# Kernel tuning notes

Measured on AMD Instinct MI355X. Metric: run time of the kernel, lower is better.

The kernel has to match this reference:

```python
import jax, jax.numpy as jnp
import numpy as np

B, T, C, HS = 4, 4096, 1024, 128

def setup_inputs() -> dict:
    key = jax.random.key(0)
    kx, kq, kk, kv = jax.random.split(key, 4)
    x = jax.random.normal(kx, (B, T, C), dtype=jnp.float32)
    # bias-free Linear weights, stored as (in, out) so projection is x @ W
    scale = 1.0 / np.sqrt(C)
    Wq = jax.random.normal(kq, (C, HS), dtype=jnp.float32) * scale
    Wk = jax.random.normal(kk, (C, HS), dtype=jnp.float32) * scale
    Wv = jax.random.normal(kv, (C, HS), dtype=jnp.float32) * scale
    return {"x": x, "Wq": Wq, "Wk": Wk, "Wv": Wv}

def reference(x, Wq, Wk, Wv):
    # x: (B,T,C) -> q,k,v: (B,T,HS)
    q = jnp.einsum('btc,ch->bth', x, Wq)
    k = jnp.einsum('btc,ch->bth', x, Wk)
    v = jnp.einsum('btc,ch->bth', x, Wv)
    hs = k.shape[-1]
    # scaled scores (B,T,T) with causal mask
    wei = jnp.einsum('bth,bsh->bts', q, k) * (hs ** -0.5)
    causal = jnp.tril(jnp.ones((q.shape[1], q.shape[1]), dtype=bool))
    wei = jnp.where(causal, wei, -jnp.inf)
    wei = jax.nn.softmax(wei, axis=-1)
    # dropout p=0.0 -> identity
    out = jnp.einsum('bts,bsh->bth', wei, v)
    return out
```

## Files before the change

### kernel.cpp

```cpp
#include <hip/hip_runtime.h>
#include <hip/hip_bf16.h>

typedef __attribute__((ext_vector_type(8))) short short8;
typedef __attribute__((ext_vector_type(4))) short s4v;
typedef __attribute__((ext_vector_type(4))) float f32x4;

#define BATCH 4
#define TLEN 4096
#define CDIM 1024
#define HSD 128
#define MROWS (BATCH*TLEN)

#define QSCALE 0.12751744f

#ifdef __HIP_DEVICE_COMPILE__
  #define MFMA16(a,b,c) __builtin_amdgcn_mfma_f32_16x16x16bf16_1k(a,b,c,0,0,0)
#else
  #define MFMA16(a,b,c) (c)
#endif

__device__ __forceinline__ unsigned short f2bf(float f){
    unsigned u = __builtin_bit_cast(unsigned, f);
    u = (u + 0x7FFFu + ((u >> 16) & 1u)) >> 16;
    return (unsigned short)u;
}
__device__ __forceinline__ unsigned pkbf(float a, float b){
    unsigned ua = (__builtin_bit_cast(unsigned, a) + 0x8000u) >> 16;
    unsigned ub = (__builtin_bit_cast(unsigned, b) + 0x8000u) & 0xFFFF0000u;
    return ua | ub;
}

__global__ void prep_w_k(const float* __restrict__ Wq, const float* __restrict__ Wk,
                         const float* __restrict__ Wv, unsigned short* __restrict__ Wt){
    int idx = blockIdx.x * 256 + threadIdx.x;
    const int total = 3 * HSD * CDIM;
    if (idx >= total) return;
    int w = idx / (HSD * CDIM);
    int r = idx - w * HSD * CDIM;
    int h = r / CDIM;
    int c = r - h * CDIM;
    const float* W = (w == 0) ? Wq : ((w == 1) ? Wk : Wv);
    Wt[idx] = f2bf(W[c * HSD + h]);
}

__device__ __forceinline__ void stage_w_tile(unsigned short* buf, const unsigned short* g,
                                             int tid){
#pragma unroll
    for (int i = 0; i < 2; i++){
        int c = i * 256 + tid;
        int row = c >> 2, kp = c & 3;
        int swz = (row & 3) ^ ((row >> 2) & 3);
        const unsigned short* gp = g + (size_t)row * CDIM + ((kp ^ swz) << 3);
        unsigned short* lp = buf + (c << 3);
        __builtin_amdgcn_global_load_lds((const __attribute__((address_space(1))) void*)gp,
                                         (__attribute__((address_space(3))) void*)lp, 16, 0, 0);
    }
}

__global__ __launch_bounds__(256) void proj_k(const float* __restrict__ x,
                                              const unsigned short* __restrict__ Wt,
                                              unsigned short* __restrict__ Qb,
                                              unsigned short* __restrict__ Kb,
                                              unsigned short* __restrict__ Vt){
    __shared__ unsigned short As[2][64 * 32];
    __shared__ unsigned short Bs[2][128 * 32];

    const int tid = threadIdx.x, lane = tid & 63, wave = tid >> 6;
    const int m = lane & 15, quad = lane >> 4;
    const int wr = wave & 1, wc = wave >> 1;
    const int rb = blockIdx.x * 64;
    const int p  = blockIdx.y;

    const float* gA = x + (size_t)rb * CDIM;
    const unsigned short* gB = Wt + (size_t)(p * HSD) * CDIM;

    const int arow = tid >> 2, ach = tid & 3;
    const int aswz = (arow & 3) ^ ((arow >> 2) & 3);
    const int agc = ach ^ aswz;
    const float* agp = gA + (size_t)arow * CDIM + (agc << 3);

    f32x4 acc[4][4];
#pragma unroll
    for (int i = 0; i < 4; i++)
#pragma unroll
        for (int j = 0; j < 4; j++) acc[i][j] = (f32x4)0.f;

    stage_w_tile(&Bs[0][0], gB, tid);
    {
        float4 a0 = *(const float4*)(agp);
        float4 a1 = *(const float4*)(agp + 4);
        short8 o;
        o[0]=(short)f2bf(a0.x); o[1]=(short)f2bf(a0.y); o[2]=(short)f2bf(a0.z); o[3]=(short)f2bf(a0.w);
        o[4]=(short)f2bf(a1.x); o[5]=(short)f2bf(a1.y); o[6]=(short)f2bf(a1.z); o[7]=(short)f2bf(a1.w);
        *(short8*)&As[0][arow * 32 + (ach << 3)] = o;
    }
    __syncthreads();

    int cur = 0;
    for (int kc = 0; kc < CDIM / 32; ++kc){
        float4 a0n, a1n;
        if (kc + 1 < CDIM / 32){
            stage_w_tile(&Bs[cur ^ 1][0], gB + (kc + 1) * 32, tid);
            a0n = *(const float4*)(agp + (kc + 1) * 32);
            a1n = *(const float4*)(agp + (kc + 1) * 32 + 4);
        }
        if (p < 2){
            short8 aF[4], bF[2];
#pragma unroll
            for (int i = 0; i < 4; i++){
                int ra = wr * 64 + i * 16 + m;
                int sa = (ra & 3) ^ ((ra >> 2) & 3);
                aF[i] = *(const short8*)&Bs[cur][ra * 32 + ((quad ^ sa) << 3)];
            }
#pragma unroll
            for (int j = 0; j < 2; j++){
                int rn = wc * 32 + j * 16 + m;
                int sb = (rn & 3) ^ ((rn >> 2) & 3);
                bF[j] = *(const short8*)&As[cur][rn * 32 + ((quad ^ sb) << 3)];
            }
#pragma unroll
            for (int i = 0; i < 4; i++)
#pragma unroll
                for (int j = 0; j < 2; j++)
                    acc[i][j] = __builtin_amdgcn_mfma_f32_16x16x32_bf16(aF[i], bF[j], acc[i][j], 0, 0, 0);
        } else {
            short8 aF[2], bF[4];
#pragma unroll
            for (int i = 0; i < 2; i++){
                int ra = wr * 32 + i * 16 + m;
                int sa = (ra & 3) ^ ((ra >> 2) & 3);
                aF[i] = *(const short8*)&As[cur][ra * 32 + ((quad ^ sa) << 3)];
            }
#pragma unroll
            for (int j = 0; j < 4; j++){
                int rn = wc * 64 + j * 16 + m;
                int sb = (rn & 3) ^ ((rn >> 2) & 3);
                bF[j] = *(const short8*)&Bs[cur][rn * 32 + ((quad ^ sb) << 3)];
            }
#pragma unroll
            for (int i = 0; i < 2; i++)
#pragma unroll
                for (int j = 0; j < 4; j++)
                    acc[i][j] = __builtin_amdgcn_mfma_f32_16x16x32_bf16(aF[i], bF[j], acc[i][j], 0, 0, 0);
        }
        if (kc + 1 < CDIM / 32){
            short8 o;
            o[0]=(short)f2bf(a0n.x); o[1]=(short)f2bf(a0n.y); o[2]=(short)f2bf(a0n.z); o[3]=(short)f2bf(a0n.w);
            o[4]=(short)f2bf(a1n.x); o[5]=(short)f2bf(a1n.y); o[6]=(short)f2bf(a1n.z); o[7]=(short)f2bf(a1n.w);
            *(short8*)&As[cur ^ 1][arow * 32 + (ach << 3)] = o;
        }
        __syncthreads();
        cur ^= 1;
    }

    if (p < 2){
        unsigned short* D = (p == 0) ? Qb : Kb;
        const float qs = (p == 0) ? QSCALE : 1.0f;
#pragma unroll
        for (int i = 0; i < 4; i++){
#pragma unroll
            for (int j = 0; j < 2; j++){
                int h = wr * 64 + i * 16 + quad * 4;
                int t = rb + wc * 32 + j * 16 + m;
                ushort4 v;
                v.x = f2bf(acc[i][j][0] * qs); v.y = f2bf(acc[i][j][1] * qs);
                v.z = f2bf(acc[i][j][2] * qs); v.w = f2bf(acc[i][j][3] * qs);
                *(ushort4*)(D + (size_t)t * HSD + h) = v;
            }
        }
    } else {
        int b = rb >> 12;
        int tb = rb & 4095;
#pragma unroll
        for (int i = 0; i < 2; i++){
#pragma unroll
            for (int j = 0; j < 4; j++){
                int t = tb + wr * 32 + i * 16 + quad * 4;
                int h = wc * 64 + j * 16 + m;
                ushort4 v;
                v.x = f2bf(acc[i][j][0]); v.y = f2bf(acc[i][j][1]);
                v.z = f2bf(acc[i][j][2]); v.w = f2bf(acc[i][j][3]);
                *(ushort4*)(Vt + ((size_t)b * HSD + h) * TLEN + t) = v;
            }
        }
    }
}

__device__ __forceinline__ void stage_k_tile(unsigned short* buf, const unsigned short* g,
                                             int tid){
#pragma unroll
    for (int i = 0; i < 2; i++){
        int slot = i * 512 + tid;
        int row = slot >> 4;
        int ch  = slot & 15;
        const unsigned short* gp = g + row * 128 + ((ch ^ (row & 15)) << 3);
        unsigned short* lp = buf + (slot << 3);
        __builtin_amdgcn_global_load_lds((const __attribute__((address_space(1))) void*)gp,
                                         (__attribute__((address_space(3))) void*)lp, 16, 0, 0);
    }
}
__device__ __forceinline__ void stage_v_tile(unsigned short* buf, const unsigned short* g,
                                             int tid){
#pragma unroll
    for (int i = 0; i < 2; i++){
        int slot = i * 512 + tid;
        int row = slot >> 3;
        int ch  = slot & 7;
        const unsigned short* gp = g + (size_t)row * TLEN + ((ch ^ (row & 7)) << 3);
        unsigned short* lp = buf + (slot << 3);
        __builtin_amdgcn_global_load_lds((const __attribute__((address_space(1))) void*)gp,
                                         (__attribute__((address_space(3))) void*)lp, 16, 0, 0);
    }
}

__global__ __launch_bounds__(512) void attn_k(const unsigned short* __restrict__ Qb,
                       const unsigned short* __restrict__ Kb,
                       const unsigned short* __restrict__ Vts,
                       float* __restrict__ Opart, float* __restrict__ lpart, int seglen){
    __shared__ unsigned short Kt[64 * 128];
    __shared__ unsigned short Vs[128 * 64];

    const int tid = threadIdx.x, lane = tid & 63, wave = tid >> 6;
    const int m = lane & 15, quad = lane >> 4;
    const int q0 = ((int)gridDim.x - 1 - (int)blockIdx.x) * 128;
    const int seg = blockIdx.y, b = blockIdx.z;
    const int g0 = seg * seglen;
    if (g0 >= q0 + 128) return;
    const int gend = min(g0 + seglen, q0 + 128);
    const int nT = (gend - g0) >> 6;

    const int q0w = q0 + wave * 16;
    const size_t rowg = (size_t)b * TLEN + q0w;

    short8 aQ[4];
#pragma unroll
    for (int kk = 0; kk < 4; kk++)
        aQ[kk] = *(const short8*)(Qb + (rowg + m) * HSD + kk * 32 + quad * 8);

    f32x4 accO[8];
#pragma unroll
    for (int i = 0; i < 8; i++) accO[i] = (f32x4)0.f;
    float lp = 0.f;

    const unsigned short* kbase = Kb + (size_t)b * TLEN * HSD;
    const unsigned short* vbase = Vts + (size_t)b * HSD * TLEN;

    for (int t = 0; t < nT; ++t){
        const int s0 = g0 + t * 64;
        stage_k_tile(&Kt[0], kbase + (size_t)s0 * HSD, tid);
        stage_v_tile(&Vs[0], vbase + s0, tid);
        __syncthreads();

        if (s0 <= q0w + 15){
            f32x4 S[4];
#pragma unroll
            for (int ns = 0; ns < 4; ns++){
                f32x4 sa = (f32x4)0.f;
#pragma unroll
                for (int kk = 0; kk < 4; kk++){
                    short8 bK = *(const short8*)&Kt[(ns * 16 + m) * 128 + (((kk * 4 + quad) ^ m) << 3)];
                    sa = __builtin_amdgcn_mfma_f32_16x16x32_bf16(bK, aQ[kk], sa, 0, 0, 0);
                }
                S[ns] = sa;
            }
            if (s0 + 63 > q0w){
                int qg = q0w + m;
#pragma unroll
                for (int ns = 0; ns < 4; ns++){
#pragma unroll
                    for (int r = 0; r < 4; r++){
                        int sg = s0 + ns * 16 + quad * 4 + r;
                        if (sg > qg) S[ns][r] = -1e30f;
                    }
                }
            }
            s4v aP[4];
#pragma unroll
            for (int ns = 0; ns < 4; ns++){
                float p0 = exp2f(S[ns][0]), p1 = exp2f(S[ns][1]);
                float p2 = exp2f(S[ns][2]), p3 = exp2f(S[ns][3]);
                lp += (p0 + p1) + (p2 + p3);
                uint2 u;
                u.x = pkbf(p0, p1);
                u.y = pkbf(p2, p3);
                aP[ns] = __builtin_bit_cast(s4v, u);
            }
#pragma unroll
            for (int sub = 0; sub < 8; sub++){
#pragma unroll
                for (int ns = 0; ns < 4; ns++){
                    s4v bV = *(const s4v*)&Vs[(sub * 16 + m) * 64 +
                            (((2 * ns + (quad >> 1)) ^ (m & 7)) << 3) + (quad & 1) * 4];
                    accO[sub] = MFMA16(aP[ns], bV, accO[sub]);
                }
            }
        }
        __syncthreads();
    }
    lp += __shfl_xor(lp, 16, 64);
    lp += __shfl_xor(lp, 32, 64);
    if (quad == 0)
        lpart[(size_t)seg * MROWS + rowg + m] = lp;
    float* ob = Opart + (size_t)seg * MROWS * HSD;
#pragma unroll
    for (int sub = 0; sub < 8; sub++)
#pragma unroll
        for (int r = 0; r < 4; r++)
            ob[(rowg + quad * 4 + r) * HSD + sub * 16 + m] = accO[sub][r];
}

__global__ void merge_k(const float* __restrict__ Opart, const float* __restrict__ lpart,
                        float* __restrict__ out, int nseg, int seglen){
    int idx = blockIdx.x * 256 + threadIdx.x;
    int row = idx >> 7;
    int t = row & (TLEN - 1);
    int q0 = t & ~127;
    int nsv = min(nseg, (q0 + 127) / seglen + 1);
    float L = 0.f, o = 0.f;
    for (int s = 0; s < nsv; s++){
        L += lpart[(size_t)s * MROWS + row];
        o += Opart[(size_t)s * MROWS * HSD + idx];
    }
    out[idx] = o / L;
}

extern "C" void kernel_launch(void* const* d_in, const int* in_sizes, int n_in,
                              void* d_out, int out_size, void* d_ws, size_t ws_size,
                              hipStream_t stream) {
    const float* x  = (const float*)d_in[0];
    const float* Wq = (const float*)d_in[1];
    const float* Wk = (const float*)d_in[2];
    const float* Wv = (const float*)d_in[3];
    float* out = (float*)d_out;
    char* w = (char*)d_ws;

    unsigned short* Wt = (unsigned short*)w;
    unsigned short* Qb = (unsigned short*)(w + ((size_t)1u  << 20));
    unsigned short* Kb = (unsigned short*)(w + ((size_t)5u  << 20));
    unsigned short* Vt = (unsigned short*)(w + ((size_t)9u  << 20));
    float* lpart       = (float*)(w + ((size_t)13u << 20));
    float* Opart;
    int nseg;
    const size_t segbytes = (size_t)MROWS * HSD * 4;
    if (ws_size >= ((size_t)14u << 20) + 8 * segbytes){
        nseg = 8;  Opart = (float*)(w + ((size_t)14u << 20));
    } else if (ws_size >= ((size_t)14u << 20) + 4 * segbytes){
        nseg = 4;  Opart = (float*)(w + ((size_t)14u << 20));
    } else {
        nseg = 1;  Opart = out;
    }
    const int seglen = TLEN / nseg;

    prep_w_k<<<(3 * HSD * CDIM + 255) / 256, 256, 0, stream>>>(Wq, Wk, Wv, Wt);
    proj_k<<<dim3(MROWS / 64, 3), 256, 0, stream>>>(x, Wt, Qb, Kb, Vt);
    attn_k<<<dim3(TLEN / 128, nseg, BATCH), 512, 0, stream>>>(Qb, Kb, Vt, Opart, lpart, seglen);
    merge_k<<<(MROWS * HSD) / 256, 256, 0, stream>>>(Opart, lpart, out, nseg, seglen);
}
```

Before: 202.6 us.

## Fuse QKV projection into one pass, double-buffer attention K/V tiles, tile weight transpose

The projection kernel now computes Q, K and V together in one 512-thread block per 64-row tile, so x is read and converted to bf16 once instead of three times. The attention kernel double-buffers its K/V LDS tiles, prefetching the next tile while computing on the current one, and raises wave priority around the MFMA sections. The weight transpose uses a shared-memory tiled transpose for coalesced access. The costs are more LDS per block, lower occupancy in the projection kernel, and scalar uncoalesced V-transpose stores.

```diff
diff --git a/kernel.cpp b/kernel.cpp
--- a/kernel.cpp
+++ b/kernel.cpp
@@ -32,22 +32,28 @@
 
 __global__ void prep_w_k(const float* __restrict__ Wq, const float* __restrict__ Wk,
                          const float* __restrict__ Wv, unsigned short* __restrict__ Wt){
-    int idx = blockIdx.x * 256 + threadIdx.x;
-    const int total = 3 * HSD * CDIM;
-    if (idx >= total) return;
-    int w = idx / (HSD * CDIM);
-    int r = idx - w * HSD * CDIM;
-    int h = r / CDIM;
-    int c = r - h * CDIM;
+    __shared__ float tile[32][33];
+    const int w = blockIdx.z;
     const float* W = (w == 0) ? Wq : ((w == 1) ? Wk : Wv);
-    Wt[idx] = f2bf(W[c * HSD + h]);
-}
-
-__device__ __forceinline__ void stage_w_tile(unsigned short* buf, const unsigned short* g,
-                                             int tid){
-#pragma unroll
-    for (int i = 0; i < 2; i++){
-        int c = i * 256 + tid;
+    const int c0 = blockIdx.x * 32, h0 = blockIdx.y * 32;
+    const int lx = threadIdx.x & 31, ly = threadIdx.x >> 5;
+#pragma unroll
+    for (int i = 0; i < 4; i++){
+        int c = c0 + ly + i * 8;
+        tile[ly + i * 8][lx] = W[(size_t)c * HSD + h0 + lx];
+    }
+    __syncthreads();
+#pragma unroll
+    for (int i = 0; i < 4; i++){
+        int h = h0 + ly + i * 8;
+        Wt[((size_t)w * HSD + h) * CDIM + c0 + lx] = f2bf(tile[lx][ly + i * 8]);
+    }
+}
+
+__device__ __forceinline__ void stage_wb(unsigned short* buf, const unsigned short* g, int tid){
+#pragma unroll
+    for (int i = 0; i < 3; i++){
+        int c = i * 512 + tid;
         int row = c >> 2, kp = c & 3;
         int swz = (row & 3) ^ ((row >> 2) & 3);
         const unsigned short* gp = g + (size_t)row * CDIM + ((kp ^ swz) << 3);
@@ -57,36 +63,35 @@
     }
 }
 
-__global__ __launch_bounds__(256) void proj_k(const float* __restrict__ x,
+__global__ __launch_bounds__(512) void proj_k(const float* __restrict__ x,
                                               const unsigned short* __restrict__ Wt,
                                               unsigned short* __restrict__ Qb,
                                               unsigned short* __restrict__ Kb,
                                               unsigned short* __restrict__ Vt){
     __shared__ unsigned short As[2][64 * 32];
-    __shared__ unsigned short Bs[2][128 * 32];
+    __shared__ unsigned short Bs[2][384 * 32];
 
     const int tid = threadIdx.x, lane = tid & 63, wave = tid >> 6;
     const int m = lane & 15, quad = lane >> 4;
-    const int wr = wave & 1, wc = wave >> 1;
+    const int wr = wave & 1;
+    const int wc = wave >> 1;
     const int rb = blockIdx.x * 64;
-    const int p  = blockIdx.y;
 
     const float* gA = x + (size_t)rb * CDIM;
-    const unsigned short* gB = Wt + (size_t)(p * HSD) * CDIM;
 
     const int arow = tid >> 2, ach = tid & 3;
     const int aswz = (arow & 3) ^ ((arow >> 2) & 3);
     const int agc = ach ^ aswz;
     const float* agp = gA + (size_t)arow * CDIM + (agc << 3);
 
-    f32x4 acc[4][4];
-#pragma unroll
-    for (int i = 0; i < 4; i++)
-#pragma unroll
-        for (int j = 0; j < 4; j++) acc[i][j] = (f32x4)0.f;
-
-    stage_w_tile(&Bs[0][0], gB, tid);
-    {
+    f32x4 acc[6][2];
+#pragma unroll
+    for (int i = 0; i < 6; i++)
+#pragma unroll
+        for (int j = 0; j < 2; j++) acc[i][j] = (f32x4)0.f;
+
+    stage_wb(&Bs[0][0], Wt, tid);
+    if (tid < 256){
         float4 a0 = *(const float4*)(agp);
         float4 a1 = *(const float4*)(agp + 4);
         short8 o;
@@ -100,50 +105,33 @@
     for (int kc = 0; kc < CDIM / 32; ++kc){
         float4 a0n, a1n;
         if (kc + 1 < CDIM / 32){
-            stage_w_tile(&Bs[cur ^ 1][0], gB + (kc + 1) * 32, tid);
-            a0n = *(const float4*)(agp + (kc + 1) * 32);
-            a1n = *(const float4*)(agp + (kc + 1) * 32 + 4);
-        }
-        if (p < 2){
-            short8 aF[4], bF[2];
-#pragma unroll
-            for (int i = 0; i < 4; i++){
-                int ra = wr * 64 + i * 16 + m;
+            stage_wb(&Bs[cur ^ 1][0], Wt + (kc + 1) * 32, tid);
+            if (tid < 256){
+                a0n = *(const float4*)(agp + (kc + 1) * 32);
+                a1n = *(const float4*)(agp + (kc + 1) * 32 + 4);
+            }
+        }
+        {
+            short8 aF[6], bF[2];
+#pragma unroll
+            for (int i = 0; i < 6; i++){
+                int ra = wc * 96 + i * 16 + m;
                 int sa = (ra & 3) ^ ((ra >> 2) & 3);
                 aF[i] = *(const short8*)&Bs[cur][ra * 32 + ((quad ^ sa) << 3)];
             }
 #pragma unroll
             for (int j = 0; j < 2; j++){
-                int rn = wc * 32 + j * 16 + m;
+                int rn = wr * 32 + j * 16 + m;
                 int sb = (rn & 3) ^ ((rn >> 2) & 3);
                 bF[j] = *(const short8*)&As[cur][rn * 32 + ((quad ^ sb) << 3)];
             }
 #pragma unroll
-            for (int i = 0; i < 4; i++)
+            for (int i = 0; i < 6; i++)
 #pragma unroll
                 for (int j = 0; j < 2; j++)
                     acc[i][j] = __builtin_amdgcn_mfma_f32_16x16x32_bf16(aF[i], bF[j], acc[i][j], 0, 0, 0);
-        } else {
-            short8 aF[2], bF[4];
-#pragma unroll
-            for (int i = 0; i < 2; i++){
-                int ra = wr * 32 + i * 16 + m;
-                int sa = (ra & 3) ^ ((ra >> 2) & 3);
-                aF[i] = *(const short8*)&As[cur][ra * 32 + ((quad ^ sa) << 3)];
-            }
-#pragma unroll
-            for (int j = 0; j < 4; j++){
-                int rn = wc * 64 + j * 16 + m;
-                int sb = (rn & 3) ^ ((rn >> 2) & 3);
-                bF[j] = *(const short8*)&Bs[cur][rn * 32 + ((quad ^ sb) << 3)];
-            }
-#pragma unroll
-            for (int i = 0; i < 2; i++)
-#pragma unroll
-                for (int j = 0; j < 4; j++)
-                    acc[i][j] = __builtin_amdgcn_mfma_f32_16x16x32_bf16(aF[i], bF[j], acc[i][j], 0, 0, 0);
-        }
-        if (kc + 1 < CDIM / 32){
+        }
+        if (kc + 1 < CDIM / 32 && tid < 256){
             short8 o;
             o[0]=(short)f2bf(a0n.x); o[1]=(short)f2bf(a0n.y); o[2]=(short)f2bf(a0n.z); o[3]=(short)f2bf(a0n.w);
             o[4]=(short)f2bf(a1n.x); o[5]=(short)f2bf(a1n.y); o[6]=(short)f2bf(a1n.z); o[7]=(short)f2bf(a1n.w);
@@ -153,34 +141,30 @@
         cur ^= 1;
     }
 
-    if (p < 2){
-        unsigned short* D = (p == 0) ? Qb : Kb;
-        const float qs = (p == 0) ? QSCALE : 1.0f;
-#pragma unroll
-        for (int i = 0; i < 4; i++){
-#pragma unroll
-            for (int j = 0; j < 2; j++){
-                int h = wr * 64 + i * 16 + quad * 4;
-                int t = rb + wc * 32 + j * 16 + m;
+    const int b = rb >> 12;
+#pragma unroll
+    for (int i = 0; i < 6; i++){
+        const int hbase = wc * 96 + i * 16;
+        const int type = hbase >> 7;
+        const int hp = hbase + quad * 4;
+#pragma unroll
+        for (int j = 0; j < 2; j++){
+            const int t = rb + wr * 32 + j * 16 + m;
+            if (type == 0){
                 ushort4 v;
-                v.x = f2bf(acc[i][j][0] * qs); v.y = f2bf(acc[i][j][1] * qs);
-                v.z = f2bf(acc[i][j][2] * qs); v.w = f2bf(acc[i][j][3] * qs);
-                *(ushort4*)(D + (size_t)t * HSD + h) = v;
-            }
-        }
-    } else {
-        int b = rb >> 12;
-        int tb = rb & 4095;
-#pragma unroll
-        for (int i = 0; i < 2; i++){
-#pragma unroll
-            for (int j = 0; j < 4; j++){
-                int t = tb + wr * 32 + i * 16 + quad * 4;
-                int h = wc * 64 + j * 16 + m;
+                v.x = f2bf(acc[i][j][0] * QSCALE); v.y = f2bf(acc[i][j][1] * QSCALE);
+                v.z = f2bf(acc[i][j][2] * QSCALE); v.w = f2bf(acc[i][j][3] * QSCALE);
+                *(ushort4*)(Qb + (size_t)t * HSD + hp) = v;
+            } else if (type == 1){
                 ushort4 v;
                 v.x = f2bf(acc[i][j][0]); v.y = f2bf(acc[i][j][1]);
                 v.z = f2bf(acc[i][j][2]); v.w = f2bf(acc[i][j][3]);
-                *(ushort4*)(Vt + ((size_t)b * HSD + h) * TLEN + t) = v;
+                *(ushort4*)(Kb + (size_t)t * HSD + (hp - 128)) = v;
+            } else {
+                const int tt = t & (TLEN - 1);
+#pragma unroll
+                for (int r = 0; r < 4; r++)
+                    Vt[((size_t)b * HSD + (hp - 256 + r)) * TLEN + tt] = f2bf(acc[i][j][r]);
             }
         }
     }
@@ -217,8 +201,8 @@
                        const unsigned short* __restrict__ Kb,
                        const unsigned short* __restrict__ Vts,
                        float* __restrict__ Opart, float* __restrict__ lpart, int seglen){
-    __shared__ unsigned short Kt[64 * 128];
-    __shared__ unsigned short Vs[128 * 64];
+    __shared__ unsigned short Kt[2][64 * 128];
+    __shared__ unsigned short Vs[2][128 * 64];
 
     const int tid = threadIdx.x, lane = tid & 63, wave = tid >> 6;
     const int m = lane & 15, quad = lane >> 4;
@@ -232,6 +216,12 @@
     const int q0w = q0 + wave * 16;
     const size_t rowg = (size_t)b * TLEN + q0w;
 
+    const unsigned short* kbase = Kb + (size_t)b * TLEN * HSD;
+    const unsigned short* vbase = Vts + (size_t)b * HSD * TLEN;
+
+    stage_k_tile(&Kt[0][0], kbase + (size_t)g0 * HSD, tid);
+    stage_v_tile(&Vs[0][0], vbase + g0, tid);
+
     short8 aQ[4];
 #pragma unroll
     for (int kk = 0; kk < 4; kk++)
@@ -242,27 +232,31 @@
     for (int i = 0; i < 8; i++) accO[i] = (f32x4)0.f;
     float lp = 0.f;
 
-    const unsigned short* kbase = Kb + (size_t)b * TLEN * HSD;
-    const unsigned short* vbase = Vts + (size_t)b * HSD * TLEN;
+    __syncthreads();
+    int cur = 0;
 
     for (int t = 0; t < nT; ++t){
         const int s0 = g0 + t * 64;
-        stage_k_tile(&Kt[0], kbase + (size_t)s0 * HSD, tid);
-        stage_v_tile(&Vs[0], vbase + s0, tid);
-        __syncthreads();
-
+        if (t + 1 < nT){
+            stage_k_tile(&Kt[cur ^ 1][0], kbase + (size_t)(s0 + 64) * HSD, tid);
+            stage_v_tile(&Vs[cur ^ 1][0], vbase + (s0 + 64), tid);
+        }
         if (s0 <= q0w + 15){
+            const unsigned short* Ktc = &Kt[cur][0];
+            const unsigned short* Vsc = &Vs[cur][0];
             f32x4 S[4];
+            __builtin_amdgcn_s_setprio(1);
 #pragma unroll
             for (int ns = 0; ns < 4; ns++){
                 f32x4 sa = (f32x4)0.f;
 #pragma unroll
                 for (int kk = 0; kk < 4; kk++){
-                    short8 bK = *(const short8*)&Kt[(ns * 16 + m) * 128 + (((kk * 4 + quad) ^ m) << 3)];
+                    short8 bK = *(const short8*)&Ktc[(ns * 16 + m) * 128 + (((kk * 4 + quad) ^ m) << 3)];
                     sa = __builtin_amdgcn_mfma_f32_16x16x32_bf16(bK, aQ[kk], sa, 0, 0, 0);
                 }
                 S[ns] = sa;
             }
+            __builtin_amdgcn_s_setprio(0);
             if (s0 + 63 > q0w){
                 int qg = q0w + m;
 #pragma unroll
@@ -285,17 +279,20 @@
                 u.y = pkbf(p2, p3);
                 aP[ns] = __builtin_bit_cast(s4v, u);
             }
+            __builtin_amdgcn_s_setprio(1);
 #pragma unroll
             for (int sub = 0; sub < 8; sub++){
 #pragma unroll
                 for (int ns = 0; ns < 4; ns++){
-                    s4v bV = *(const s4v*)&Vs[(sub * 16 + m) * 64 +
+                    s4v bV = *(const s4v*)&Vsc[(sub * 16 + m) * 64 +
                             (((2 * ns + (quad >> 1)) ^ (m & 7)) << 3) + (quad & 1) * 4];
                     accO[sub] = MFMA16(aP[ns], bV, accO[sub]);
                 }
             }
+            __builtin_amdgcn_s_setprio(0);
         }
         __syncthreads();
+        cur ^= 1;
     }
     lp += __shfl_xor(lp, 16, 64);
     lp += __shfl_xor(lp, 32, 64);
@@ -351,8 +348,8 @@
     }
     const int seglen = TLEN / nseg;
 
-    prep_w_k<<<(3 * HSD * CDIM + 255) / 256, 256, 0, stream>>>(Wq, Wk, Wv, Wt);
-    proj_k<<<dim3(MROWS / 64, 3), 256, 0, stream>>>(x, Wt, Qb, Kb, Vt);
+    prep_w_k<<<dim3(CDIM / 32, HSD / 32, 3), 256, 0, stream>>>(Wq, Wk, Wv, Wt);
+    proj_k<<<dim3(MROWS / 64), 512, 0, stream>>>(x, Wt, Qb, Kb, Vt);
     attn_k<<<dim3(TLEN / 128, nseg, BATCH), 512, 0, stream>>>(Qb, Kb, Vt, Opart, lpart, seglen);
     merge_k<<<(MROWS * HSD) / 256, 256, 0, stream>>>(Opart, lpart, out, nseg, seglen);
 }
```

Result: no change. 199.7 us (-1.5%).
